# Kernel optimization log

Hardware: AMD Instinct MI355X
Metric: run time of the kernel (lower is better)

## Reference

```python
import jax, jax.numpy as jnp
import numpy as np

EPS = 1e-5  # BatchNorm eps (inference mode, running_mean=0, running_var=1)

def conv3(x, w, b=None):
    y = jax.lax.conv_general_dilated(x, w, (1, 1), ((1, 1), (1, 1)),
                                     dimension_numbers=('NCHW', 'OIHW', 'NCHW'))
    if b is not None:
        y = y + b[None, :, None, None]
    return y

def bn(x, g):
    # g: [2, C] = (gamma, beta); eval-mode BN with running stats (0, 1)
    scale = (g[0] / jnp.sqrt(1.0 + EPS))[None, :, None, None]
    return x * scale + g[1][None, :, None, None]

def bcr(x, w, g, b=None):  # BasicConv2d: conv -> BN -> ReLU
    return jax.nn.relu(bn(conv3(x, w, b), g))

def setup_inputs() -> dict:
    key = jax.random.key(0)
    B, ch1, ch2, H, W = 2, 64, 128, 64, 64
    ks = jax.random.split(key, 16)
    w = lambda k, o, i: (jax.random.normal(k, (o, i, 3, 3), jnp.float32) * 0.05)
    g = lambda c: jnp.stack([jnp.ones((c,), jnp.float32), jnp.zeros((c,), jnp.float32)])
    return {
        'xs': jax.random.normal(ks[0], (B, ch1, H, W), jnp.float32),
        'xc': jax.random.normal(ks[1], (B, ch2, H, W), jnp.float32),
        'w_g1': w(ks[2], 32, ch1), 'g_g1': g(32),
        'w_g2': w(ks[3], 32, ch2), 'g_g2': g(32),
        'w_ls': w(ks[4], ch1, ch1 + 32), 'b_ls': jnp.zeros((ch1,), jnp.float32), 'g_ls': g(ch1),
        'w_lc': w(ks[5], ch2, ch2 + 32), 'b_lc': jnp.zeros((ch2,), jnp.float32), 'g_lc': g(ch2),
        'w_c1': w(ks[6], 32, ch1), 'g_c1': g(32),
        'w_c2': w(ks[7], 32, ch2), 'g_c2': g(32),
        'w_o1': w(ks[8], ch1, ch1), 'g_o1': g(ch1),
        'w_o2': w(ks[9], ch2, ch2), 'g_o2': g(ch2),
        'w_oa': w(ks[10], 1, 1), 'g_oa': g(1),
    }

def reference(xs, xc, w_g1, g_g1, w_g2, g_g2, w_ls, b_ls, g_ls,
              w_lc, b_lc, g_lc, w_c1, g_c1, w_c2, g_c2,
              w_o1, g_o1, w_o2, g_o2, w_oa, g_oa):
    B, ch1, H, W = xs.shape
    ch2 = xc.shape[1]
    N = H * W
    # global context: conv+BN+ReLU -> GAP (1x1) -> bilinear upsample from 1x1 == broadcast
    g_s = jnp.mean(bcr(xs, w_g1, g_g1), axis=(2, 3), keepdims=True)  # [B,32,1,1]
    g_c = jnp.mean(bcr(xc, w_g2, g_g2), axis=(2, 3), keepdims=True)
    gs = jnp.broadcast_to(g_s, (B, 32, H, W))
    gc = jnp.broadcast_to(g_c, (B, 32, H, W))
    xs1 = jax.nn.relu(bn(conv3(jnp.concatenate([gs, xs], axis=1), w_ls, b_ls), g_ls)) + xs
    xc1 = jax.nn.relu(bn(conv3(jnp.concatenate([gc, xc], axis=1), w_lc, b_lc), g_lc)) + xc
    # dual cross-spatial attention
    fs = bcr(xs1, w_c1, g_c1).reshape(B, 32, N)
    fc = bcr(xc1, w_c2, g_c2).reshape(B, 32, N)
    att = jnp.einsum('bcn,bcm->bnm', fs, fc)  # [B,N,N]
    sm_cols = jax.nn.softmax(att, axis=-2)    # softmax over n (rows)
    sm_rows = jax.nn.softmax(att, axis=-1)    # softmax over m
    outs = jnp.einsum('bcn,bnm->bcm', xs1.reshape(B, ch1, N), sm_cols).reshape(B, ch1, H, W)
    # xc_flat @ softmax(att^T, -2): (att^T).softmax(-2)[m,j] = sm_rows[j,m]
    outc = jnp.einsum('bcm,bjm->bcj', xc1.reshape(B, ch2, N), sm_rows).reshape(B, ch2, H, W)
    out_s = bcr(outs, w_o1, g_o1) + xs1
    out_c = bcr(outc, w_o2, g_o2) + xc1
    att2 = att + jnp.swapaxes(att, -1, -2)
    att3 = jax.nn.softmax(att2, axis=-2) + jnp.swapaxes(jax.nn.softmax(att2, axis=-1), -1, -2)
    att_map = bcr(att3[:, None], w_oa, g_oa)  # [B,1,N,N]
    return (att_map, out_s, out_c, g_s, g_c)
```

## Files before the change

kernel.cpp:

```cpp
#include <hip/hip_runtime.h>


#define LB __launch_bounds__(256)

constexpr float BN_SCALE = 0.99999500003749968f;
constexpr float NEG_BIG  = -3.402823466e38f;
constexpr float LOG2E    = 1.4426950408889634f;
constexpr float LN2      = 0.6931471805599453f;

typedef __attribute__((ext_vector_type(8))) short short8v;
typedef __attribute__((ext_vector_type(4))) float f32x4;

__device__ __forceinline__ ushort bf16rne(float f) {
    unsigned u = __float_as_uint(f);
    unsigned r = (u + 0x7FFFu + ((u >> 16) & 1u)) >> 16;
    return (ushort)r;
}
__device__ __forceinline__ float bf2f(ushort u) {
    return __uint_as_float((unsigned)u << 16);
}

__device__ __forceinline__ void online_merge(float& mx, float& sm, float m2, float s2) {
    const float mn = fmaxf(mx, m2);
    sm = sm * __expf(mx - mn) + s2 * __expf(m2 - mn);
    mx = mn;
}

__global__ LB void transpose_bf(const float* __restrict__ in, ushort* __restrict__ outT,
                                int C, int HW)
{
    __shared__ float t[32][33];
    const int tid = threadIdx.x;
    const int tx = tid & 31, ty0 = tid >> 5;
    const int hw0 = blockIdx.x * 32, c0 = blockIdx.y * 32, b = blockIdx.z;
    #pragma unroll
    for (int i = 0; i < 4; ++i)
        t[ty0 + i * 8][tx] = in[((long)b * C + c0 + ty0 + i * 8) * HW + hw0 + tx];
    __syncthreads();
    #pragma unroll
    for (int i = 0; i < 4; ++i)
        outT[((long)b * HW + hw0 + ty0 + i * 8) * C + c0 + tx] =
            bf16rne(t[tx][ty0 + i * 8]);
}

template<int HASG, int OCB>
__global__ LB void conv3x3_mfma(
    const ushort* __restrict__ inT,
    const float* __restrict__ gconst,
    const float* __restrict__ w,
    const float* __restrict__ bias,
    const float* __restrict__ bn,
    const float* __restrict__ residual,
    float* __restrict__ out,
    ushort* __restrict__ outbf,
    ushort* __restrict__ outTbf,
    int Cg, int Cin, int Cout)
{
    constexpr int TILES = OCB / 16;
    constexpr int TPO = 256 / OCB;
    constexpr int J = 288 / TPO;
    __shared__ ushort ldsA[9][OCB][36];
    __shared__ float wg[OCB][10];
    const int tid = threadIdx.x;
    const int wv = tid >> 6, lane = tid & 63;
    const int fr = lane & 15, fg = lane >> 4;
    const int px0 = blockIdx.x * 64, ocb = blockIdx.y * OCB, b = blockIdx.z;
    const int Ct = Cg + Cin;
    const int p = px0 + wv * 16 + fr;
    const int y = p >> 6, x = p & 63;

    if (HASG) {
        for (int e = tid; e < OCB * 9; e += 256) {
            const int oc = e / 9, k = e % 9;
            float s = 0.f;
            for (int ic = 0; ic < Cg; ++ic)
                s += gconst[b * Cg + ic] * w[((long)(ocb + oc) * Ct + ic) * 9 + k];
            wg[oc][k] = s;
        }
    }

    int qv[9]; bool val[9];
    #pragma unroll
    for (int k = 0; k < 9; ++k) {
        const int yy = y + k / 3 - 1, xx = x + k % 3 - 1;
        val[k] = ((unsigned)yy < 64u) && ((unsigned)xx < 64u);
        qv[k] = val[k] ? (yy * 64 + xx) : 0;
    }

    f32x4 acc[TILES];
    #pragma unroll
    for (int t = 0; t < TILES; ++t) acc[t] = (f32x4){0.f, 0.f, 0.f, 0.f};
    const short8v bz = (short8v){0, 0, 0, 0, 0, 0, 0, 0};

    const int oc_st = tid / TPO, q = tid % TPO;
    const int base_ic = q * (J / 9);
    const ushort* inTb = inT + (long)b * 4096 * Cin + 8 * fg;

    const int NCH = Cin / 32;
    for (int c = 0; c < NCH; ++c) {
        __syncthreads();
        {
            const float* wp = w + (long)(ocb + oc_st) * Ct * 9
                              + (long)(Cg + c * 32) * 9 + q * J;
            #pragma unroll
            for (int j4 = 0; j4 < J; j4 += 4) {
                const float4 v4 = *(const float4*)&wp[j4];
                ldsA[(j4 + 0) % 9][oc_st][base_ic + (j4 + 0) / 9] = bf16rne(v4.x);
                ldsA[(j4 + 1) % 9][oc_st][base_ic + (j4 + 1) / 9] = bf16rne(v4.y);
                ldsA[(j4 + 2) % 9][oc_st][base_ic + (j4 + 2) / 9] = bf16rne(v4.z);
                ldsA[(j4 + 3) % 9][oc_st][base_ic + (j4 + 3) / 9] = bf16rne(v4.w);
            }
        }
        __syncthreads();
        const ushort* inc = inTb + c * 32;
        #pragma unroll
        for (int k = 0; k < 9; ++k) {
            const short8v bfrag = val[k] ? *(const short8v*)&inc[(long)qv[k] * Cin] : bz;
            #pragma unroll
            for (int t = 0; t < TILES; ++t) {
                const short8v afrag = *(const short8v*)&ldsA[k][t * 16 + fr][8 * fg];
                acc[t] = __builtin_amdgcn_mfma_f32_16x16x32_bf16(afrag, bfrag, acc[t], 0, 0, 0);
            }
        }
    }

    #pragma unroll
    for (int t = 0; t < TILES; ++t) {
        float v4[4];
        #pragma unroll
        for (int r = 0; r < 4; ++r) {
            const int ocl = t * 16 + fg * 4 + r;
            const int oc = ocb + ocl;
            float v = acc[t][r];
            if (bias) v += bias[oc];
            if (HASG) {
                #pragma unroll
                for (int k = 0; k < 9; ++k)
                    if (val[k]) v += wg[ocl][k];
            }
            v = fmaxf(fmaf(v, bn[oc] * BN_SCALE, bn[Cout + oc]), 0.f);
            const long oidx = ((long)(b * Cout + oc)) * 4096 + p;
            if (residual) v += residual[oidx];
            out[oidx] = v;
            if (outbf) outbf[oidx] = bf16rne(v);
            v4[r] = v;
        }
        if (outTbf) {
            ushort4 o;
            o.x = bf16rne(v4[0]); o.y = bf16rne(v4[1]);
            o.z = bf16rne(v4[2]); o.w = bf16rne(v4[3]);
            *(ushort4*)&outTbf[((long)(b * 4096 + p)) * Cout + ocb + t * 16 + fg * 4] = o;
        }
    }
}

__global__ LB void gap_kernel(const float* __restrict__ in,
                              float* __restrict__ o1, float* __restrict__ o2,
                              int C, int HW)
{
    const int c = blockIdx.x, b = blockIdx.y;
    const float* p = in + ((long)b * C + c) * HW;
    float s = 0.f;
    for (int i = threadIdx.x; i < HW; i += 256) s += p[i];
    #pragma unroll
    for (int off = 32; off; off >>= 1) s += __shfl_down(s, off);
    __shared__ float red[4];
    if ((threadIdx.x & 63) == 0) red[threadIdx.x >> 6] = s;
    __syncthreads();
    if (threadIdx.x == 0) {
        const float t = (red[0] + red[1] + red[2] + red[3]) / (float)HW;
        o1[b * C + c] = t;
        o2[b * C + c] = t;
    }
}

__global__ LB void att_gemm(const float* __restrict__ fs, const float* __restrict__ fc,
                            float* __restrict__ att, float* __restrict__ attT, int N)
{
    __shared__ float lfs[32][33];
    const int tid = threadIdx.x;
    const int m  = blockIdx.x * 256 + tid;
    const int n0 = blockIdx.y * 32;
    const int b  = blockIdx.z;
    for (int i = tid; i < 1024; i += 256) {
        const int c = i >> 5, nn = i & 31;
        lfs[c][nn] = fs[((long)b * 32 + c) * N + n0 + nn];
    }
    __syncthreads();
    float acc[32];
    #pragma unroll
    for (int i = 0; i < 32; ++i) acc[i] = 0.f;
    const float* fcp = fc + (long)b * 32 * N + m;
    #pragma unroll
    for (int c = 0; c < 32; ++c) {
        const float f = fcp[(long)c * N];
        #pragma unroll
        for (int nn = 0; nn < 32; ++nn) acc[nn] = fmaf(lfs[c][nn], f, acc[nn]);
    }
    float* op = att + ((long)b * N + n0) * N + m;
    #pragma unroll
    for (int nn = 0; nn < 32; ++nn) op[(long)nn * N] = acc[nn];
    float* opT = attT + ((long)b * N + m) * N + n0;
    #pragma unroll
    for (int q = 0; q < 8; ++q)
        *(float4*)&opT[q * 4] = make_float4(acc[q*4], acc[q*4+1], acc[q*4+2], acc[q*4+3]);
}

__global__ LB void tri_stats(const float* __restrict__ att, const float* __restrict__ attT,
                             ushort* __restrict__ att2bf,
                             float* __restrict__ McP, float* __restrict__ ScP,
                             float* __restrict__ MrP, float* __restrict__ SrP,
                             float* __restrict__ M2P, float* __restrict__ S2P, int N)
{
    __shared__ float lm[3][4][64], ls[3][4][64];
    const int c = threadIdx.x & 63, q = threadIdx.x >> 6;
    const int m = blockIdx.x * 64 + c;
    const int y = blockIdx.y, b = blockIdx.z;
    const long base = (long)b * N * N + ((long)y * 128 + q) * N + m;

    float av[32], tv[32];
    #pragma unroll
    for (int r = 0; r < 32; ++r) {
        const long off = base + (long)r * 4 * N;
        av[r] = att[off];
        tv[r] = attT[off];
        att2bf[off] = bf16rne(av[r] + tv[r]);
    }
    float mc = av[0], mr = tv[0], m2 = av[0] + tv[0];
    #pragma unroll
    for (int r = 1; r < 32; ++r) {
        mc = fmaxf(mc, av[r]);
        mr = fmaxf(mr, tv[r]);
        m2 = fmaxf(m2, av[r] + tv[r]);
    }
    const float mcL = mc * LOG2E, mrL = mr * LOG2E, m2L = m2 * LOG2E;
    float sc = 0.f, sr = 0.f, s2 = 0.f;
    #pragma unroll
    for (int r = 0; r < 32; ++r) {
        sc += exp2f(fmaf(av[r], LOG2E, -mcL));
        sr += exp2f(fmaf(tv[r], LOG2E, -mrL));
        s2 += exp2f(fmaf(av[r] + tv[r], LOG2E, -m2L));
    }

    lm[0][q][c] = mc; ls[0][q][c] = sc;
    lm[1][q][c] = mr; ls[1][q][c] = sr;
    lm[2][q][c] = m2; ls[2][q][c] = s2;
    __syncthreads();
    if (q < 3) {
        float M = lm[q][0][c], S = ls[q][0][c];
        #pragma unroll
        for (int j = 1; j < 4; ++j) online_merge(M, S, lm[q][j][c], ls[q][j][c]);
        float* Pm = (q == 0) ? McP : ((q == 1) ? MrP : M2P);
        float* Ps = (q == 0) ? ScP : ((q == 1) ? SrP : S2P);
        Pm[((long)(b * 32 + y)) * N + m] = M;
        Ps[((long)(b * 32 + y)) * N + m] = S;
    }
}

__global__ LB void stats_comb32(const float* __restrict__ Mp, const float* __restrict__ Sp,
                                float* __restrict__ M, float* __restrict__ Sm,
                                float* __restrict__ C2L, int N)
{
    __shared__ float lm[4][64], ls[4][64];
    const int c = threadIdx.x & 63, q = threadIdx.x >> 6;
    const int n = blockIdx.x * 64 + c;
    const int b = blockIdx.y;
    float mx = NEG_BIG, sum = 0.f;
    #pragma unroll
    for (int j = 0; j < 8; ++j) {
        const int s = q * 8 + j;
        online_merge(mx, sum, Mp[((long)(b * 32 + s)) * N + n], Sp[((long)(b * 32 + s)) * N + n]);
    }
    lm[q][c] = mx; ls[q][c] = sum;
    __syncthreads();
    if (q == 0) {
        #pragma unroll
        for (int j = 1; j < 4; ++j) online_merge(mx, sum, lm[j][c], ls[j][c]);
        M[(long)b * N + n]  = mx;
        Sm[(long)b * N + n] = sum;
        if (C2L) C2L[(long)b * N + n] = (mx - LN2 + __logf(sum)) * LOG2E;
    }
}

template<int MROWS>
__global__ LB void sm_gemm_mfma(const ushort* __restrict__ Xbf,
                                const float* __restrict__ A,
                                const float* __restrict__ Mv,
                                float* __restrict__ parts,
                                int N)
{
    constexpr int RT = MROWS / 32;
    constexpr int AR_SH = (MROWS == 128) ? 1 : 2;
    constexpr int ALD = (MROWS == 128) ? 4 : 2;
    __shared__ ushort ldsA[MROWS][80];
    __shared__ ushort ldsB[32][80];

    const int tid = threadIdx.x;
    const int wave = tid >> 6, lane = tid & 63;
    const int col0 = blockIdx.x * 32;
    const int s = blockIdx.y, b = blockIdx.z;
    const int KLEN = N / 4, K0 = s * KLEN;

    const int scol = tid >> 3, sq = tid & 7;
    const int ar = tid >> AR_SH;
    const int ak = (tid & ((1 << AR_SH) - 1)) * (ALD * 8);
    const int wct = wave & 1, wrh = wave >> 1;
    const int fr = lane & 15, fg = lane >> 4;

    f32x4 acc[RT];
    #pragma unroll
    for (int i = 0; i < RT; ++i) acc[i] = (f32x4){0.f, 0.f, 0.f, 0.f};

    const float* ab = A + ((long)b * N + col0) * N + (long)scol * N + K0 + sq * 8;
    const ushort* xb = Xbf + (long)b * MROWS * N + (long)ar * N + K0 + ak;
    const float mvl = Mv[(long)b * N + col0 + scol] * LOG2E;

    float4 bv0 = *(const float4*)&ab[0];
    float4 bv1 = *(const float4*)&ab[4];
    short8v av[ALD];
    #pragma unroll
    for (int j = 0; j < ALD; ++j) av[j] = *(const short8v*)&xb[8 * j];

    const int NIT = KLEN / 64;
    for (int it = 0; it < NIT; ++it) {
        __syncthreads();
        ushort4 o0, o1;
        o0.x = bf16rne(exp2f(fmaf(bv0.x, LOG2E, -mvl)));
        o0.y = bf16rne(exp2f(fmaf(bv0.y, LOG2E, -mvl)));
        o0.z = bf16rne(exp2f(fmaf(bv0.z, LOG2E, -mvl)));
        o0.w = bf16rne(exp2f(fmaf(bv0.w, LOG2E, -mvl)));
        o1.x = bf16rne(exp2f(fmaf(bv1.x, LOG2E, -mvl)));
        o1.y = bf16rne(exp2f(fmaf(bv1.y, LOG2E, -mvl)));
        o1.z = bf16rne(exp2f(fmaf(bv1.z, LOG2E, -mvl)));
        o1.w = bf16rne(exp2f(fmaf(bv1.w, LOG2E, -mvl)));
        *(ushort4*)&ldsB[scol][sq * 8] = o0;
        *(ushort4*)&ldsB[scol][sq * 8 + 4] = o1;
        #pragma unroll
        for (int j = 0; j < ALD; ++j) *(short8v*)&ldsA[ar][ak + 8 * j] = av[j];
        __syncthreads();
        if (it + 1 < NIT) {
            const int kb = (it + 1) * 64;
            bv0 = *(const float4*)&ab[kb];
            bv1 = *(const float4*)&ab[kb + 4];
            #pragma unroll
            for (int j = 0; j < ALD; ++j)
                av[j] = *(const short8v*)&xb[kb + 8 * j];
        }
        #pragma unroll
        for (int kk = 0; kk < 2; ++kk) {
            const short8v bfrag = *(const short8v*)&ldsB[wct * 16 + fr][32 * kk + 8 * fg];
            #pragma unroll
            for (int rt = 0; rt < RT; ++rt) {
                const int row = wrh * (MROWS / 2) + rt * 16 + fr;
                const short8v afrag = *(const short8v*)&ldsA[row][32 * kk + 8 * fg];
                acc[rt] = __builtin_amdgcn_mfma_f32_16x16x32_bf16(afrag, bfrag, acc[rt], 0, 0, 0);
            }
        }
    }

    float* pp = parts + ((long)(s * 2 + b) * MROWS) * N;
    #pragma unroll
    for (int rt = 0; rt < RT; ++rt) {
        #pragma unroll
        for (int r = 0; r < 4; ++r) {
            const int row = wrh * (MROWS / 2) + rt * 16 + fg * 4 + r;
            const int col = col0 + wct * 16 + fr;
            pp[(long)row * N + col] = acc[rt][r];
        }
    }
}

template<int C>
__global__ LB void sm_reduce4(const float* __restrict__ parts,
                              const float* __restrict__ denom, float* __restrict__ outp, int N)
{
    const long idx = (long)blockIdx.x * 256 + threadIdx.x;
    const int m = (int)(idx & (long)(N - 1));
    const long bc = idx >> 12;
    const int c = (int)(bc & (C - 1));
    const int b = (int)(bc / C);
    float s = 0.f;
    #pragma unroll
    for (int ss = 0; ss < 4; ++ss)
        s += parts[((long)(ss * 2 + b) * C + c) * N + m];
    outp[idx] = s / denom[(long)b * N + m];
}

__global__ LB void attmap_conv(const ushort* __restrict__ att2bf,
                               const float* __restrict__ C2L,
                               const float* __restrict__ w, const float* __restrict__ g,
                               float* __restrict__ out, int N)
{
    __shared__ float tD[34][136];
    __shared__ float ldc[130];
    const int tid = threadIdx.x;
    const int x0 = (blockIdx.x & 31) * 128;
    const int y0 = (blockIdx.x >> 5) * 32;
    const int b = blockIdx.y;
    const ushort* ap = att2bf + (long)b * N * N;
    const float* cp = C2L + (long)b * N;

    if (tid < 130) {
        const int xx = x0 + tid - 1;
        ldc[tid] = ((unsigned)xx < (unsigned)N) ? cp[xx] : 0.f;
    }
    __syncthreads();

    {
        const int xg = (tid & 31) * 4;
        const int rg = tid >> 5;
        #pragma unroll
        for (int i = 0; i < 5; ++i) {
            const int hy = rg + i * 8;
            if (hy < 34) {
                const int yy = y0 + hy - 1;
                float4 v = make_float4(0.f, 0.f, 0.f, 0.f);
                if ((unsigned)yy < (unsigned)N) {
                    const ushort4 a = *(const ushort4*)&ap[(long)yy * N + x0 + xg];
                    v.x = exp2f(fmaf(bf2f(a.x), LOG2E, -ldc[xg + 1]));
                    v.y = exp2f(fmaf(bf2f(a.y), LOG2E, -ldc[xg + 2]));
                    v.z = exp2f(fmaf(bf2f(a.z), LOG2E, -ldc[xg + 3]));
                    v.w = exp2f(fmaf(bf2f(a.w), LOG2E, -ldc[xg + 4]));
                }
                *(float4*)&tD[hy][xg + 4] = v;
            }
        }
    }
    if (tid < 68) {
        const int c01 = tid & 1, hy = tid >> 1;
        const int col = c01 ? 132 : 3;
        const int xx = c01 ? (x0 + 128) : (x0 - 1);
        const int yy = y0 + hy - 1;
        float v = 0.f;
        if ((unsigned)yy < (unsigned)N && (unsigned)xx < (unsigned)N)
            v = exp2f(fmaf(bf2f(ap[(long)yy * N + xx]), LOG2E, -ldc[c01 ? 129 : 0]));
        tD[hy][col] = v;
    }
    __syncthreads();

    const float scale = g[0] * BN_SCALE, beta = g[1];
    const int tx2 = tid & 127, tyg = tid >> 7;
    float* ob = out + (long)b * N * N + (long)y0 * N + x0 + tx2;
    #pragma unroll
    for (int rr = 0; rr < 16; ++rr) {
        const int ly = tyg + rr * 2;
        float acc = 0.f;
        #pragma unroll
        for (int ky = 0; ky < 3; ++ky)
            #pragma unroll
            for (int kx = 0; kx < 3; ++kx)
                acc = fmaf(w[ky * 3 + kx], tD[ly + ky][tx2 + 3 + kx], acc);
        ob[(long)ly * N] = fmaxf(fmaf(acc, scale, beta), 0.f);
    }
}

extern "C" void kernel_launch(void* const* d_in, const int* in_sizes, int n_in,
                              void* d_out, int out_size, void* d_ws, size_t ws_size,
                              hipStream_t stream)
{
    const float* xs   = (const float*)d_in[0];
    const float* xc   = (const float*)d_in[1];
    const float* w_g1 = (const float*)d_in[2];
    const float* g_g1 = (const float*)d_in[3];
    const float* w_g2 = (const float*)d_in[4];
    const float* g_g2 = (const float*)d_in[5];
    const float* w_ls = (const float*)d_in[6];
    const float* b_ls = (const float*)d_in[7];
    const float* g_ls = (const float*)d_in[8];
    const float* w_lc = (const float*)d_in[9];
    const float* b_lc = (const float*)d_in[10];
    const float* g_lc = (const float*)d_in[11];
    const float* w_c1 = (const float*)d_in[12];
    const float* g_c1 = (const float*)d_in[13];
    const float* w_c2 = (const float*)d_in[14];
    const float* g_c2 = (const float*)d_in[15];
    const float* w_o1 = (const float*)d_in[16];
    const float* g_o1 = (const float*)d_in[17];
    const float* w_o2 = (const float*)d_in[18];
    const float* g_o2 = (const float*)d_in[19];
    const float* w_oa = (const float*)d_in[20];
    const float* g_oa = (const float*)d_in[21];

    const int B = 2, HW = 4096, N = 4096;

    float* ws = (float*)d_ws;
    float* xs1    = ws;
    float* xc1    = ws + 524288;
    float* fs     = ws + 1572864;
    float* fc     = ws + 1835008;
    float* t32    = ws + 2097152;
    float* McP    = ws + 1572864;
    float* ScP    = ws + 1835008;
    float* MrP    = ws + 2097152;
    float* SrP    = ws + 2359296;
    float* M2P    = ws + 2621440;
    float* S2P    = ws + 2883584;
    float* outs_w = ws + 2359296;
    float* outc_w = ws + 2883584;
    float* gs_w   = ws + 3932160;
    float* gc_w   = ws + 3932224;
    float* Mc     = ws + 3932288;
    float* Sc     = ws + 3940480;
    float* Mr     = ws + 3948672;
    float* Sr     = ws + 3956864;
    float* M2     = ws + 3965056;
    float* S2     = ws + 3973248;
    float* C2L    = ws + 3981440;
    float* att    = ws + 4243584;
    float* attT   = ws + 37798016;
    float* pg     = ws + 71352448;
    ushort* att2bf = (ushort*)(ws + 75546752);

    float* out = (float*)d_out;
    float* out_attmap = out;
    ushort* xs1bf   = (ushort*)out;
    ushort* xc1bf   = (ushort*)(out + 262144);
    ushort* xcT     = (ushort*)(out + 786432);
    ushort* outcT   = (ushort*)(out + 786432);
    ushort* xsT     = (ushort*)(out + 1310720);
    ushort* outs_wT = (ushort*)(out + 1310720);
    ushort* xs1T    = (ushort*)(out + 1572864);
    ushort* xc1T    = (ushort*)(out + 1835008);
    float* out_s      = out + 33554432;
    float* out_c      = out + 34078720;
    float* out_gs     = out + 35127296;
    float* out_gc     = out + 35127360;

    const dim3 blk(256);

    transpose_bf<<<dim3(128, 2, B), blk, 0, stream>>>(xs, xsT, 64, HW);
    transpose_bf<<<dim3(128, 4, B), blk, 0, stream>>>(xc, xcT, 128, HW);
    conv3x3_mfma<0, 32><<<dim3(64, 1, B), blk, 0, stream>>>(xsT, nullptr, w_g1, nullptr, g_g1, nullptr, t32, nullptr, nullptr, 0, 64, 32);
    gap_kernel<<<dim3(32, B), blk, 0, stream>>>(t32, gs_w, out_gs, 32, HW);
    conv3x3_mfma<0, 32><<<dim3(64, 1, B), blk, 0, stream>>>(xcT, nullptr, w_g2, nullptr, g_g2, nullptr, t32, nullptr, nullptr, 0, 128, 32);
    gap_kernel<<<dim3(32, B), blk, 0, stream>>>(t32, gc_w, out_gc, 32, HW);
    conv3x3_mfma<1, 64><<<dim3(64, 1, B), blk, 0, stream>>>(xsT, gs_w, w_ls, b_ls, g_ls, xs, xs1, xs1bf, xs1T, 32, 64, 64);
    conv3x3_mfma<1, 64><<<dim3(64, 2, B), blk, 0, stream>>>(xcT, gc_w, w_lc, b_lc, g_lc, xc, xc1, xc1bf, xc1T, 32, 128, 128);
    conv3x3_mfma<0, 32><<<dim3(64, 1, B), blk, 0, stream>>>(xs1T, nullptr, w_c1, nullptr, g_c1, nullptr, fs, nullptr, nullptr, 0, 64, 32);
    conv3x3_mfma<0, 32><<<dim3(64, 1, B), blk, 0, stream>>>(xc1T, nullptr, w_c2, nullptr, g_c2, nullptr, fc, nullptr, nullptr, 0, 128, 32);
    att_gemm<<<dim3(16, 128, B), blk, 0, stream>>>(fs, fc, att, attT, N);
    tri_stats<<<dim3(64, 32, B), blk, 0, stream>>>(att, attT, att2bf, McP, ScP, MrP, SrP, M2P, S2P, N);
    stats_comb32<<<dim3(64, B), blk, 0, stream>>>(McP, ScP, Mc, Sc, nullptr, N);
    stats_comb32<<<dim3(64, B), blk, 0, stream>>>(MrP, SrP, Mr, Sr, nullptr, N);
    stats_comb32<<<dim3(64, B), blk, 0, stream>>>(M2P, S2P, M2, S2, C2L, N);
    sm_gemm_mfma<128><<<dim3(128, 4, B), blk, 0, stream>>>(xc1bf, att, Mr, pg, N);
    sm_reduce4<128><<<dim3((B * 128 * N) / 256), blk, 0, stream>>>(pg, Sr, outc_w, N);
    transpose_bf<<<dim3(128, 4, B), blk, 0, stream>>>(outc_w, outcT, 128, HW);
    conv3x3_mfma<0, 64><<<dim3(64, 2, B), blk, 0, stream>>>(outcT, nullptr, w_o2, nullptr, g_o2, xc1, out_c, nullptr, nullptr, 0, 128, 128);
    sm_gemm_mfma<64><<<dim3(128, 4, B), blk, 0, stream>>>(xs1bf, attT, Mc, pg, N);
    sm_reduce4<64><<<dim3((B * 64 * N) / 256), blk, 0, stream>>>(pg, Sc, outs_w, N);
    transpose_bf<<<dim3(128, 2, B), blk, 0, stream>>>(outs_w, outs_wT, 64, HW);
    conv3x3_mfma<0, 64><<<dim3(64, 1, B), blk, 0, stream>>>(outs_wT, nullptr, w_o1, nullptr, g_o1, xs1, out_s, nullptr, nullptr, 0, 64, 64);
    attmap_conv<<<dim3(4096, B), blk, 0, stream>>>(att2bf, C2L, w_oa, g_oa, out_attmap, N);
}
```

Baseline: 518.5 us.

## Fuse attention-score statistics and bf16 sum into the attention GEMM

The separate tri_stats pass, which reread both full N×N att and attT matrices, is removed. Instead the GEMM kernel also computes the transposed product tile in registers and emits the bf16 att+attT values plus per-32-row max/sum partials for the three softmaxes. The cost is doubled FMA work and register pressure in the GEMM, and four times more partial statistics that stats_comb must merge. Those partials move to a new workspace region.

```diff
diff --git a/kernel.cpp b/kernel.cpp
--- a/kernel.cpp
+++ b/kernel.cpp
@@ -174,108 +174,96 @@
     }
 }
 
-__global__ LB void att_gemm(const float* __restrict__ fs, const float* __restrict__ fc,
-                            float* __restrict__ att, float* __restrict__ attT, int N)
-{
-    __shared__ float lfs[32][33];
+__global__ LB void att_gemm2(const float* __restrict__ fs, const float* __restrict__ fc,
+                             float* __restrict__ att, float* __restrict__ attT,
+                             ushort* __restrict__ att2bf,
+                             float* __restrict__ McP, float* __restrict__ ScP,
+                             float* __restrict__ MrP, float* __restrict__ SrP,
+                             float* __restrict__ M2P, float* __restrict__ S2P, int N)
+{
+    __shared__ float lfs[32][33], lfc[32][33];
     const int tid = threadIdx.x;
     const int m  = blockIdx.x * 256 + tid;
-    const int n0 = blockIdx.y * 32;
+    const int j  = blockIdx.y;
+    const int n0 = j * 32;
     const int b  = blockIdx.z;
     for (int i = tid; i < 1024; i += 256) {
         const int c = i >> 5, nn = i & 31;
         lfs[c][nn] = fs[((long)b * 32 + c) * N + n0 + nn];
+        lfc[c][nn] = fc[((long)b * 32 + c) * N + n0 + nn];
     }
     __syncthreads();
-    float acc[32];
-    #pragma unroll
-    for (int i = 0; i < 32; ++i) acc[i] = 0.f;
+    float accA[32], accB[32];
+    #pragma unroll
+    for (int i = 0; i < 32; ++i) { accA[i] = 0.f; accB[i] = 0.f; }
     const float* fcp = fc + (long)b * 32 * N + m;
+    const float* fsp = fs + (long)b * 32 * N + m;
     #pragma unroll
     for (int c = 0; c < 32; ++c) {
-        const float f = fcp[(long)c * N];
-        #pragma unroll
-        for (int nn = 0; nn < 32; ++nn) acc[nn] = fmaf(lfs[c][nn], f, acc[nn]);
+        const float vc = fcp[(long)c * N];
+        const float vs = fsp[(long)c * N];
+        #pragma unroll
+        for (int nn = 0; nn < 32; ++nn) {
+            accA[nn] = fmaf(lfs[c][nn], vc, accA[nn]);
+            accB[nn] = fmaf(lfc[c][nn], vs, accB[nn]);
+        }
     }
     float* op = att + ((long)b * N + n0) * N + m;
     #pragma unroll
-    for (int nn = 0; nn < 32; ++nn) op[(long)nn * N] = acc[nn];
+    for (int nn = 0; nn < 32; ++nn) op[(long)nn * N] = accA[nn];
     float* opT = attT + ((long)b * N + m) * N + n0;
     #pragma unroll
     for (int q = 0; q < 8; ++q)
-        *(float4*)&opT[q * 4] = make_float4(acc[q*4], acc[q*4+1], acc[q*4+2], acc[q*4+3]);
-}
-
-__global__ LB void tri_stats(const float* __restrict__ att, const float* __restrict__ attT,
-                             ushort* __restrict__ att2bf,
-                             float* __restrict__ McP, float* __restrict__ ScP,
-                             float* __restrict__ MrP, float* __restrict__ SrP,
-                             float* __restrict__ M2P, float* __restrict__ S2P, int N)
-{
-    __shared__ float lm[3][4][64], ls[3][4][64];
-    const int c = threadIdx.x & 63, q = threadIdx.x >> 6;
-    const int m = blockIdx.x * 64 + c;
-    const int y = blockIdx.y, b = blockIdx.z;
-    const long base = (long)b * N * N + ((long)y * 128 + q) * N + m;
-
-    float av[32], tv[32];
-    #pragma unroll
-    for (int r = 0; r < 32; ++r) {
-        const long off = base + (long)r * 4 * N;
-        av[r] = att[off];
-        tv[r] = attT[off];
-        att2bf[off] = bf16rne(av[r] + tv[r]);
-    }
-    float mc = av[0], mr = tv[0], m2 = av[0] + tv[0];
-    #pragma unroll
-    for (int r = 1; r < 32; ++r) {
-        mc = fmaxf(mc, av[r]);
-        mr = fmaxf(mr, tv[r]);
-        m2 = fmaxf(m2, av[r] + tv[r]);
+        *(float4*)&opT[q * 4] = make_float4(accA[q*4], accA[q*4+1], accA[q*4+2], accA[q*4+3]);
+    ushort* o2 = att2bf + ((long)b * N + m) * N + n0;
+    #pragma unroll
+    for (int q = 0; q < 8; ++q) {
+        ushort4 u;
+        u.x = bf16rne(accA[q*4+0] + accB[q*4+0]);
+        u.y = bf16rne(accA[q*4+1] + accB[q*4+1]);
+        u.z = bf16rne(accA[q*4+2] + accB[q*4+2]);
+        u.w = bf16rne(accA[q*4+3] + accB[q*4+3]);
+        *(ushort4*)&o2[q * 4] = u;
+    }
+    float mc = accA[0], mr = accB[0], m2 = accA[0] + accB[0];
+    #pragma unroll
+    for (int nn = 1; nn < 32; ++nn) {
+        mc = fmaxf(mc, accA[nn]);
+        mr = fmaxf(mr, accB[nn]);
+        m2 = fmaxf(m2, accA[nn] + accB[nn]);
     }
     const float mcL = mc * LOG2E, mrL = mr * LOG2E, m2L = m2 * LOG2E;
     float sc = 0.f, sr = 0.f, s2 = 0.f;
     #pragma unroll
-    for (int r = 0; r < 32; ++r) {
-        sc += exp2f(fmaf(av[r], LOG2E, -mcL));
-        sr += exp2f(fmaf(tv[r], LOG2E, -mrL));
-        s2 += exp2f(fmaf(av[r] + tv[r], LOG2E, -m2L));
-    }
-
-    lm[0][q][c] = mc; ls[0][q][c] = sc;
-    lm[1][q][c] = mr; ls[1][q][c] = sr;
-    lm[2][q][c] = m2; ls[2][q][c] = s2;
-    __syncthreads();
-    if (q < 3) {
-        float M = lm[q][0][c], S = ls[q][0][c];
-        #pragma unroll
-        for (int j = 1; j < 4; ++j) online_merge(M, S, lm[q][j][c], ls[q][j][c]);
-        float* Pm = (q == 0) ? McP : ((q == 1) ? MrP : M2P);
-        float* Ps = (q == 0) ? ScP : ((q == 1) ? SrP : S2P);
-        Pm[((long)(b * 32 + y)) * N + m] = M;
-        Ps[((long)(b * 32 + y)) * N + m] = S;
-    }
-}
-
-__global__ LB void stats_comb32(const float* __restrict__ Mp, const float* __restrict__ Sp,
-                                float* __restrict__ M, float* __restrict__ Sm,
-                                float* __restrict__ C2L, int N)
+    for (int nn = 0; nn < 32; ++nn) {
+        sc += exp2f(fmaf(accA[nn], LOG2E, -mcL));
+        sr += exp2f(fmaf(accB[nn], LOG2E, -mrL));
+        s2 += exp2f(fmaf(accA[nn] + accB[nn], LOG2E, -m2L));
+    }
+    const long sidx = ((long)(b * 128 + j)) * N + m;
+    McP[sidx] = mc; ScP[sidx] = sc;
+    MrP[sidx] = mr; SrP[sidx] = sr;
+    M2P[sidx] = m2; S2P[sidx] = s2;
+}
+
+__global__ LB void stats_comb128(const float* __restrict__ Mp, const float* __restrict__ Sp,
+                                 float* __restrict__ M, float* __restrict__ Sm,
+                                 float* __restrict__ C2L, int N)
 {
     __shared__ float lm[4][64], ls[4][64];
     const int c = threadIdx.x & 63, q = threadIdx.x >> 6;
     const int n = blockIdx.x * 64 + c;
     const int b = blockIdx.y;
     float mx = NEG_BIG, sum = 0.f;
-    #pragma unroll
-    for (int j = 0; j < 8; ++j) {
-        const int s = q * 8 + j;
-        online_merge(mx, sum, Mp[((long)(b * 32 + s)) * N + n], Sp[((long)(b * 32 + s)) * N + n]);
+    for (int jj = 0; jj < 32; ++jj) {
+        const int s = q * 32 + jj;
+        online_merge(mx, sum, Mp[((long)(b * 128 + s)) * N + n], Sp[((long)(b * 128 + s)) * N + n]);
     }
     lm[q][c] = mx; ls[q][c] = sum;
     __syncthreads();
     if (q == 0) {
         #pragma unroll
-        for (int j = 1; j < 4; ++j) online_merge(mx, sum, lm[j][c], ls[j][c]);
+        for (int jj = 1; jj < 4; ++jj) online_merge(mx, sum, lm[jj][c], ls[jj][c]);
         M[(long)b * N + n]  = mx;
         Sm[(long)b * N + n] = sum;
         if (C2L) C2L[(long)b * N + n] = (mx - LN2 + __logf(sum)) * LOG2E;
@@ -489,12 +477,6 @@
     float* fs     = ws + 1572864;
     float* fc     = ws + 1835008;
     float* t32    = ws + 2097152;
-    float* McP    = ws + 1572864;
-    float* ScP    = ws + 1835008;
-    float* MrP    = ws + 2097152;
-    float* SrP    = ws + 2359296;
-    float* M2P    = ws + 2621440;
-    float* S2P    = ws + 2883584;
     float* outs_w = ws + 2359296;
     float* outc_w = ws + 2883584;
     float* gs_w   = ws + 3932160;
@@ -510,6 +492,12 @@
     float* attT   = ws + 37798016;
     float* pg     = ws + 71352448;
     ushort* att2bf = (ushort*)(ws + 75546752);
+    float* McP    = ws + 92323968;
+    float* ScP    = ws + 93372544;
+    float* MrP    = ws + 94421120;
+    float* SrP    = ws + 95469696;
+    float* M2P    = ws + 96518272;
+    float* S2P    = ws + 97566848;
 
     float* out = (float*)d_out;
     float* out_attmap = out;
@@ -538,11 +526,11 @@
     conv3x3_mfma<1, 64><<<dim3(64, 2, B), blk, 0, stream>>>(xcT, gc_w, w_lc, b_lc, g_lc, xc, xc1, xc1bf, xc1T, 32, 128, 128);
     conv3x3_mfma<0, 32><<<dim3(64, 1, B), blk, 0, stream>>>(xs1T, nullptr, w_c1, nullptr, g_c1, nullptr, fs, nullptr, nullptr, 0, 64, 32);
     conv3x3_mfma<0, 32><<<dim3(64, 1, B), blk, 0, stream>>>(xc1T, nullptr, w_c2, nullptr, g_c2, nullptr, fc, nullptr, nullptr, 0, 128, 32);
-    att_gemm<<<dim3(16, 128, B), blk, 0, stream>>>(fs, fc, att, attT, N);
-    tri_stats<<<dim3(64, 32, B), blk, 0, stream>>>(att, attT, att2bf, McP, ScP, MrP, SrP, M2P, S2P, N);
-    stats_comb32<<<dim3(64, B), blk, 0, stream>>>(McP, ScP, Mc, Sc, nullptr, N);
-    stats_comb32<<<dim3(64, B), blk, 0, stream>>>(MrP, SrP, Mr, Sr, nullptr, N);
-    stats_comb32<<<dim3(64, B), blk, 0, stream>>>(M2P, S2P, M2, S2, C2L, N);
+    att_gemm2<<<dim3(16, 128, B), blk, 0, stream>>>(fs, fc, att, attT, att2bf,
+                                                    McP, ScP, MrP, SrP, M2P, S2P, N);
+    stats_comb128<<<dim3(64, B), blk, 0, stream>>>(McP, ScP, Mc, Sc, nullptr, N);
+    stats_comb128<<<dim3(64, B), blk, 0, stream>>>(MrP, SrP, Mr, Sr, nullptr, N);
+    stats_comb128<<<dim3(64, B), blk, 0, stream>>>(M2P, S2P, M2, S2, C2L, N);
     sm_gemm_mfma<128><<<dim3(128, 4, B), blk, 0, stream>>>(xc1bf, att, Mr, pg, N);
     sm_reduce4<128><<<dim3((B * 128 * N) / 256), blk, 0, stream>>>(pg, Sr, outc_w, N);
     transpose_bf<<<dim3(128, 4, B), blk, 0, stream>>>(outc_w, outcT, 128, HW);
```

Result: slower. 653.8 us (+26.1%).
